# Kernel tuning notes

Measured on AMD Instinct MI355X. Metric: run time of the kernel, lower is better.

Reference implementation:

```python
import jax, jax.numpy as jnp
import numpy as np


def _avgpool(x, k):
    # x: (N, C, H, W), k divides H and W
    if k == 1:
        return x
    N, C, H, W = x.shape
    return x.reshape(N, C, H // k, k, W // k, k).mean(axis=(3, 5))


def _pairwise_sum(mu1, var1, mu2, var2):
    # mu*, var*: (N, D). Broadcast to (N, N, D), fused elementwise chain + full sum.
    d = mu1[:, None, :] - mu2[None, :, :]
    v = var1[:, None, :] + var2[None, :, :]
    return jnp.sum(jnp.exp(-0.5 * d * d / v) / jnp.sqrt(v))


def setup_inputs() -> dict:
    key = jax.random.key(0)
    k1, k2, k3, k4 = jax.random.split(key, 4)
    shape = (64, 16, 64, 64)
    return {
        "mu_a": jax.random.normal(k1, shape, dtype=jnp.float32),
        "logvar_a": jax.random.normal(k2, shape, dtype=jnp.float32),
        "mu_b": jax.random.normal(k3, shape, dtype=jnp.float32),
        "logvar_b": jax.random.normal(k4, shape, dtype=jnp.float32),
        "kern": 2,
    }


def reference(mu_a, logvar_a, mu_b, logvar_b, kern):
    k2 = float(kern * kern)
    mu_a_p = _avgpool(mu_a, kern)
    mu_b_p = _avgpool(mu_b, kern)
    var_a = _avgpool(jnp.exp(logvar_a), kern) / k2
    var_b = _avgpool(jnp.exp(logvar_b), kern) / k2

    N = mu_a_p.shape[0]
    mu_a_f = mu_a_p.reshape(N, -1)
    mu_b_f = mu_b_p.reshape(N, -1)
    var_a_f = var_a.reshape(N, -1)
    var_b_f = var_b.reshape(N, -1)

    vaa = _pairwise_sum(mu_a_f, var_a_f, mu_a_f, var_a_f)
    vab = _pairwise_sum(mu_a_f, var_a_f, mu_b_f, var_b_f)
    vbb = _pairwise_sum(mu_b_f, var_b_f, mu_b_f, var_b_f)
    return vaa + vbb - 2.0 * vab
```

## Files before the change

kernel.cpp:

```cpp
#include <hip/hip_runtime.h>

#define N_ 64
#define C_ 16
#define H_ 64
#define W_ 64

#define TRI_BLOCKS 288
#define PAIR_GROUPS (2 * TRI_BLOCKS + 512)
#define DSPLIT 4
#define PAIR_BLOCKS (PAIR_GROUPS * DSPLIT)


__global__ __launch_bounds__(256) void pool_kernel(
    const float* __restrict__ mu_a, const float* __restrict__ lv_a,
    const float* __restrict__ mu_b, const float* __restrict__ lv_b,
    const int* __restrict__ kern_p, float* __restrict__ ws,
    float* __restrict__ out) {
    if (blockIdx.x == 0 && threadIdx.x == 0) out[0] = 0.0f;

    const int k = kern_p[0];
    const float LOG2E = 1.44269504088896f;

    if (k == 2) {
        const int Np = (N_ * C_ * H_ * W_) >> 2;
        const int Q  = Np >> 2;
        const int total = 4 * Q;
        for (int g = blockIdx.x * blockDim.x + threadIdx.x; g < total;
             g += gridDim.x * blockDim.x) {
            const int a  = g >> 18;
            const int r4 = g & (Q - 1);
            const int pw4 = (r4 & 7) << 2;
            const int t   = r4 >> 3;
            const int ph  = t & 31;
            const int nc  = t >> 5;
            const float* src = (a == 0) ? mu_a : (a == 1) ? lv_a : (a == 2) ? mu_b : lv_b;
            const bool is_var = (a & 1);
            const float* p0 = src + nc * (H_ * W_) + (ph * 2) * W_ + pw4 * 2;
            float4 r0a = *(const float4*)(p0);
            float4 r0b = *(const float4*)(p0 + 4);
            float4 r1a = *(const float4*)(p0 + W_);
            float4 r1b = *(const float4*)(p0 + W_ + 4);
            float o0, o1, o2, o3;
            if (is_var) {
#define E_(x) __builtin_amdgcn_exp2f((x) * LOG2E)
                o0 = E_(r0a.x) + E_(r0a.y) + E_(r1a.x) + E_(r1a.y);
                o1 = E_(r0a.z) + E_(r0a.w) + E_(r1a.z) + E_(r1a.w);
                o2 = E_(r0b.x) + E_(r0b.y) + E_(r1b.x) + E_(r1b.y);
                o3 = E_(r0b.z) + E_(r0b.w) + E_(r1b.z) + E_(r1b.w);
#undef E_
                const float s = 1.0f / 16.0f;
                o0 *= s; o1 *= s; o2 *= s; o3 *= s;
            } else {
                o0 = r0a.x + r0a.y + r1a.x + r1a.y;
                o1 = r0a.z + r0a.w + r1a.z + r1a.w;
                o2 = r0b.x + r0b.y + r1b.x + r1b.y;
                o3 = r0b.z + r0b.w + r1b.z + r1b.w;
                const float s = 0.25f;
                o0 *= s; o1 *= s; o2 *= s; o3 *= s;
            }
            *(float4*)(ws + (size_t)a * Np + (size_t)r4 * 4) = make_float4(o0, o1, o2, o3);
        }
    } else {
        const int Hp = H_ / k, Wp = W_ / k;
        const int Np = N_ * C_ * Hp * Wp;
        const float inv_k2 = 1.0f / (float)(k * k);
        const float inv_k4 = inv_k2 * inv_k2;
        const int total = 4 * Np;
        for (int p = blockIdx.x * blockDim.x + threadIdx.x; p < total;
             p += gridDim.x * blockDim.x) {
            const int a  = p / Np;
            const int r  = p - a * Np;
            const int pw = r % Wp;
            const int t1 = r / Wp;
            const int ph = t1 % Hp;
            const int nc = t1 / Hp;
            const float* src = (a == 0) ? mu_a : (a == 1) ? lv_a : (a == 2) ? mu_b : lv_b;
            const bool is_var = (a & 1);
            const int base = nc * (H_ * W_) + (ph * k) * W_ + (pw * k);
            float s = 0.0f;
            for (int dy = 0; dy < k; ++dy) {
                const float* row = src + base + dy * W_;
                for (int dx = 0; dx < k; ++dx) {
                    float x = row[dx];
                    s += is_var ? __builtin_amdgcn_exp2f(x * LOG2E) : x;
                }
            }
            ws[(size_t)a * Np + r] = s * (is_var ? inv_k4 : inv_k2);
        }
    }
}

__global__ __launch_bounds__(256) void pair_kernel(const float* __restrict__ ws,
                                                   const int* __restrict__ kern_p,
                                                   float* __restrict__ out) {
    const int k = kern_p[0];
    const int D  = C_ * (H_ / k) * (W_ / k);
    const int Np = N_ * D;

    const float* mu_a = ws;
    const float* va   = ws + (size_t)Np;
    const float* mu_b = ws + (size_t)2 * Np;
    const float* vb   = ws + (size_t)3 * Np;

    const int pb = blockIdx.x >> 2;
    const int c  = blockIdx.x & 3;
    int set, i, jt;
    if (pb >= 2 * TRI_BLOCKS) {
        set = 2;
        const int t = pb - 2 * TRI_BLOCKS;
        i  = t >> 3;
        jt = t & 7;
    } else {
        set = (pb >= TRI_BLOCKS) ? 1 : 0;
        const int t = (pb >= TRI_BLOCKS) ? (pb - TRI_BLOCKS) : pb;
        int g = 0;
        while (g < 7 && 4 * (g + 1) * (g + 2) <= t) ++g;
        const int r = t - 4 * g * (g + 1);
        i  = 8 * g + r / (g + 1);
        jt = r % (g + 1);
    }

    const float *mu1, *v1, *mu2, *v2;
    if (set == 0)      { mu1 = mu2 = mu_a; v1 = v2 = va; }
    else if (set == 1) { mu1 = mu2 = mu_b; v1 = v2 = vb; }
    else               { mu1 = mu_a; v1 = va; mu2 = mu_b; v2 = vb; }

    const int j0 = jt * 8;
    float wgt[8];
    for (int j8 = 0; j8 < 8; ++j8) {
        if (set == 2) wgt[j8] = -2.0f;
        else {
            const int j = j0 + j8;
            wgt[j8] = (j > i) ? 0.0f : (j == i) ? 1.0f : 2.0f;
        }
    }

    const float NHALF_LOG2E = -0.721347520444482f;
#define TERM(mx1, sx1, mx2, sx2)                                       \
    {                                                                  \
        float v  = (sx1) + (sx2);                                      \
        float rs = __builtin_amdgcn_rsqf(v);                           \
        float d  = (mx1) - (mx2);                                      \
        float t_ = d * rs;                                             \
        float e  = __builtin_amdgcn_exp2f((NHALF_LOG2E * t_) * t_);    \
        a = fmaf(e, rs, a);                                            \
    }

    float accs[8] = {0, 0, 0, 0, 0, 0, 0, 0};

    if (D == 16384) {
        const int base = (c << 12) + (threadIdx.x << 2);
        const float* Mi = mu1 + (size_t)i * D + base;
        const float* Vi = v1  + (size_t)i * D + base;
        const float4 im0 = *(const float4*)(Mi);
        const float4 im1 = *(const float4*)(Mi + 1024);
        const float4 im2 = *(const float4*)(Mi + 2048);
        const float4 im3 = *(const float4*)(Mi + 3072);
        const float4 iv0 = *(const float4*)(Vi);
        const float4 iv1 = *(const float4*)(Vi + 1024);
        const float4 iv2 = *(const float4*)(Vi + 2048);
        const float4 iv3 = *(const float4*)(Vi + 3072);
        for (int j8 = 0; j8 < 8; ++j8) {
            const float* Mj = mu2 + (size_t)(j0 + j8) * D + base;
            const float* Vj = v2  + (size_t)(j0 + j8) * D + base;
            const float4 jm0 = *(const float4*)(Mj);
            const float4 jm1 = *(const float4*)(Mj + 1024);
            const float4 jm2 = *(const float4*)(Mj + 2048);
            const float4 jm3 = *(const float4*)(Mj + 3072);
            const float4 jv0 = *(const float4*)(Vj);
            const float4 jv1 = *(const float4*)(Vj + 1024);
            const float4 jv2 = *(const float4*)(Vj + 2048);
            const float4 jv3 = *(const float4*)(Vj + 3072);
            float a = 0.0f;
            TERM(im0.x, iv0.x, jm0.x, jv0.x) TERM(im0.y, iv0.y, jm0.y, jv0.y)
            TERM(im0.z, iv0.z, jm0.z, jv0.z) TERM(im0.w, iv0.w, jm0.w, jv0.w)
            TERM(im1.x, iv1.x, jm1.x, jv1.x) TERM(im1.y, iv1.y, jm1.y, jv1.y)
            TERM(im1.z, iv1.z, jm1.z, jv1.z) TERM(im1.w, iv1.w, jm1.w, jv1.w)
            TERM(im2.x, iv2.x, jm2.x, jv2.x) TERM(im2.y, iv2.y, jm2.y, jv2.y)
            TERM(im2.z, iv2.z, jm2.z, jv2.z) TERM(im2.w, iv2.w, jm2.w, jv2.w)
            TERM(im3.x, iv3.x, jm3.x, jv3.x) TERM(im3.y, iv3.y, jm3.y, jv3.y)
            TERM(im3.z, iv3.z, jm3.z, jv3.z) TERM(im3.w, iv3.w, jm3.w, jv3.w)
            accs[j8] += a;
        }
    } else {
        const int lo = (c * D) >> 2, hi = ((c + 1) * D) >> 2;
        const float* Mi = mu1 + (size_t)i * D;
        const float* Vi = v1  + (size_t)i * D;
        for (int j8 = 0; j8 < 8; ++j8) {
            const float* Mj = mu2 + (size_t)(j0 + j8) * D;
            const float* Vj = v2  + (size_t)(j0 + j8) * D;
            float a = 0.0f;
            for (int e = lo + (int)threadIdx.x; e < hi; e += 256) {
                TERM(Mi[e], Vi[e], Mj[e], Vj[e])
            }
            accs[j8] = a;
        }
    }
#undef TERM

    float tot = 0.0f;
    for (int j8 = 0; j8 < 8; ++j8) tot += wgt[j8] * accs[j8];

    for (int off = 32; off > 0; off >>= 1)
        tot += __shfl_down(tot, off, 64);
    __shared__ float wsum[4];
    const int lane = threadIdx.x & 63;
    const int wid  = threadIdx.x >> 6;
    if (lane == 0) wsum[wid] = tot;
    __syncthreads();
    if (threadIdx.x == 0) {
        atomicAdd(out, wsum[0] + wsum[1] + wsum[2] + wsum[3]);
    }
}

extern "C" void kernel_launch(void* const* d_in, const int* in_sizes, int n_in,
                              void* d_out, int out_size, void* d_ws, size_t ws_size,
                              hipStream_t stream) {
    const float* mu_a = (const float*)d_in[0];
    const float* lv_a = (const float*)d_in[1];
    const float* mu_b = (const float*)d_in[2];
    const float* lv_b = (const float*)d_in[3];
    const int*   kern = (const int*)d_in[4];
    float* out = (float*)d_out;
    float* ws  = (float*)d_ws;

    pool_kernel<<<4096, 256, 0, stream>>>(mu_a, lv_a, mu_b, lv_b, kern, ws, out);
    pair_kernel<<<PAIR_BLOCKS, 256, 0, stream>>>(ws, kern, out);
}
```

Baseline: 165.1 us.

## Tile pair kernel as 4x8 row blocks with finer D chunking

Reworks the pairwise kernel so each block computes a 4-row by 8-column tile of sample pairs over a 1024-element chunk of the feature dimension (16 chunks), in place of one row against 8 columns over a quarter of D. Each loaded j vector is reused across four i rows, which cuts global/L2 traffic per term, and the triangular tile enumeration is recomputed for 4x8 tiles. The cost is more accumulator registers (32 per thread) and some wasted work on diagonal tiles whose upper-triangle entries get zero weight.

```diff
diff --git a/kernel.cpp b/kernel.cpp
--- a/kernel.cpp
+++ b/kernel.cpp
@@ -5,10 +5,10 @@
 #define H_ 64
 #define W_ 64
 
-#define TRI_BLOCKS 288
-#define PAIR_GROUPS (2 * TRI_BLOCKS + 512)
-#define DSPLIT 4
-#define PAIR_BLOCKS (PAIR_GROUPS * DSPLIT)
+#define TRI_TILES 72
+#define TILES 272
+#define DCHUNKS 16
+#define PAIR_BLOCKS (TILES * DCHUNKS)
 
 
 __global__ __launch_bounds__(256) void pool_kernel(
@@ -102,104 +102,99 @@
     const float* mu_b = ws + (size_t)2 * Np;
     const float* vb   = ws + (size_t)3 * Np;
 
-    const int pb = blockIdx.x >> 2;
-    const int c  = blockIdx.x & 3;
-    int set, i, jt;
-    if (pb >= 2 * TRI_BLOCKS) {
+    const int c = blockIdx.x & (DCHUNKS - 1);
+    const int t = blockIdx.x >> 4;
+    int set, it, jt;
+    if (t >= 2 * TRI_TILES) {
         set = 2;
-        const int t = pb - 2 * TRI_BLOCKS;
-        i  = t >> 3;
-        jt = t & 7;
+        const int tt = t - 2 * TRI_TILES;
+        it = tt >> 3;
+        jt = tt & 7;
     } else {
-        set = (pb >= TRI_BLOCKS) ? 1 : 0;
-        const int t = (pb >= TRI_BLOCKS) ? (pb - TRI_BLOCKS) : pb;
-        int g = 0;
-        while (g < 7 && 4 * (g + 1) * (g + 2) <= t) ++g;
-        const int r = t - 4 * g * (g + 1);
-        i  = 8 * g + r / (g + 1);
-        jt = r % (g + 1);
-    }
+        set = (t >= TRI_TILES) ? 1 : 0;
+        const int tt = set ? (t - TRI_TILES) : t;
+        int g = 0, cum = 0;
+        while (cum + (g >> 1) + 1 <= tt) { cum += (g >> 1) + 1; ++g; }
+        it = g;
+        jt = tt - cum;
+    }
+    const int i0 = it * 4, j0 = jt * 8;
 
     const float *mu1, *v1, *mu2, *v2;
     if (set == 0)      { mu1 = mu2 = mu_a; v1 = v2 = va; }
     else if (set == 1) { mu1 = mu2 = mu_b; v1 = v2 = vb; }
     else               { mu1 = mu_a; v1 = va; mu2 = mu_b; v2 = vb; }
 
-    const int j0 = jt * 8;
-    float wgt[8];
-    for (int j8 = 0; j8 < 8; ++j8) {
-        if (set == 2) wgt[j8] = -2.0f;
-        else {
-            const int j = j0 + j8;
-            wgt[j8] = (j > i) ? 0.0f : (j == i) ? 1.0f : 2.0f;
-        }
-    }
-
     const float NHALF_LOG2E = -0.721347520444482f;
-#define TERM(mx1, sx1, mx2, sx2)                                       \
+#define TERM(acc, mx1, sx1, mx2, sx2)                                  \
     {                                                                  \
         float v  = (sx1) + (sx2);                                      \
         float rs = __builtin_amdgcn_rsqf(v);                           \
         float d  = (mx1) - (mx2);                                      \
         float t_ = d * rs;                                             \
         float e  = __builtin_amdgcn_exp2f((NHALF_LOG2E * t_) * t_);    \
-        a = fmaf(e, rs, a);                                            \
-    }
-
-    float accs[8] = {0, 0, 0, 0, 0, 0, 0, 0};
+        acc = fmaf(e, rs, acc);                                        \
+    }
+
+    float accs[4][8];
+    #pragma unroll
+    for (int ir = 0; ir < 4; ++ir)
+        #pragma unroll
+        for (int j8 = 0; j8 < 8; ++j8) accs[ir][j8] = 0.0f;
 
     if (D == 16384) {
-        const int base = (c << 12) + (threadIdx.x << 2);
-        const float* Mi = mu1 + (size_t)i * D + base;
-        const float* Vi = v1  + (size_t)i * D + base;
-        const float4 im0 = *(const float4*)(Mi);
-        const float4 im1 = *(const float4*)(Mi + 1024);
-        const float4 im2 = *(const float4*)(Mi + 2048);
-        const float4 im3 = *(const float4*)(Mi + 3072);
-        const float4 iv0 = *(const float4*)(Vi);
-        const float4 iv1 = *(const float4*)(Vi + 1024);
-        const float4 iv2 = *(const float4*)(Vi + 2048);
-        const float4 iv3 = *(const float4*)(Vi + 3072);
+        const int base = (c << 10) + ((int)threadIdx.x << 2);
+        float4 im[4], iv[4];
+        #pragma unroll
+        for (int ir = 0; ir < 4; ++ir) {
+            im[ir] = *(const float4*)(mu1 + (size_t)(i0 + ir) * 16384 + base);
+            iv[ir] = *(const float4*)(v1  + (size_t)(i0 + ir) * 16384 + base);
+        }
+        #pragma unroll
         for (int j8 = 0; j8 < 8; ++j8) {
-            const float* Mj = mu2 + (size_t)(j0 + j8) * D + base;
-            const float* Vj = v2  + (size_t)(j0 + j8) * D + base;
-            const float4 jm0 = *(const float4*)(Mj);
-            const float4 jm1 = *(const float4*)(Mj + 1024);
-            const float4 jm2 = *(const float4*)(Mj + 2048);
-            const float4 jm3 = *(const float4*)(Mj + 3072);
-            const float4 jv0 = *(const float4*)(Vj);
-            const float4 jv1 = *(const float4*)(Vj + 1024);
-            const float4 jv2 = *(const float4*)(Vj + 2048);
-            const float4 jv3 = *(const float4*)(Vj + 3072);
-            float a = 0.0f;
-            TERM(im0.x, iv0.x, jm0.x, jv0.x) TERM(im0.y, iv0.y, jm0.y, jv0.y)
-            TERM(im0.z, iv0.z, jm0.z, jv0.z) TERM(im0.w, iv0.w, jm0.w, jv0.w)
-            TERM(im1.x, iv1.x, jm1.x, jv1.x) TERM(im1.y, iv1.y, jm1.y, jv1.y)
-            TERM(im1.z, iv1.z, jm1.z, jv1.z) TERM(im1.w, iv1.w, jm1.w, jv1.w)
-            TERM(im2.x, iv2.x, jm2.x, jv2.x) TERM(im2.y, iv2.y, jm2.y, jv2.y)
-            TERM(im2.z, iv2.z, jm2.z, jv2.z) TERM(im2.w, iv2.w, jm2.w, jv2.w)
-            TERM(im3.x, iv3.x, jm3.x, jv3.x) TERM(im3.y, iv3.y, jm3.y, jv3.y)
-            TERM(im3.z, iv3.z, jm3.z, jv3.z) TERM(im3.w, iv3.w, jm3.w, jv3.w)
-            accs[j8] += a;
+            const float4 jm = *(const float4*)(mu2 + (size_t)(j0 + j8) * 16384 + base);
+            const float4 jv = *(const float4*)(v2  + (size_t)(j0 + j8) * 16384 + base);
+            #pragma unroll
+            for (int ir = 0; ir < 4; ++ir) {
+                TERM(accs[ir][j8], im[ir].x, iv[ir].x, jm.x, jv.x)
+                TERM(accs[ir][j8], im[ir].y, iv[ir].y, jm.y, jv.y)
+                TERM(accs[ir][j8], im[ir].z, iv[ir].z, jm.z, jv.z)
+                TERM(accs[ir][j8], im[ir].w, iv[ir].w, jm.w, jv.w)
+            }
         }
     } else {
-        const int lo = (c * D) >> 2, hi = ((c + 1) * D) >> 2;
-        const float* Mi = mu1 + (size_t)i * D;
-        const float* Vi = v1  + (size_t)i * D;
+        const int cs = D / DCHUNKS;
+        const int lo = c * cs, hi = lo + cs;
+        for (int e = lo + (int)threadIdx.x; e < hi; e += 256) {
+            #pragma unroll
+            for (int j8 = 0; j8 < 8; ++j8) {
+                const float mj = mu2[(size_t)(j0 + j8) * D + e];
+                const float vj = v2 [(size_t)(j0 + j8) * D + e];
+                #pragma unroll
+                for (int ir = 0; ir < 4; ++ir) {
+                    const float mi = mu1[(size_t)(i0 + ir) * D + e];
+                    const float vi = v1 [(size_t)(i0 + ir) * D + e];
+                    TERM(accs[ir][j8], mi, vi, mj, vj)
+                }
+            }
+        }
+    }
+#undef TERM
+
+    float tot = 0.0f;
+    #pragma unroll
+    for (int ir = 0; ir < 4; ++ir) {
+        #pragma unroll
         for (int j8 = 0; j8 < 8; ++j8) {
-            const float* Mj = mu2 + (size_t)(j0 + j8) * D;
-            const float* Vj = v2  + (size_t)(j0 + j8) * D;
-            float a = 0.0f;
-            for (int e = lo + (int)threadIdx.x; e < hi; e += 256) {
-                TERM(Mi[e], Vi[e], Mj[e], Vj[e])
-            }
-            accs[j8] = a;
-        }
-    }
-#undef TERM
-
-    float tot = 0.0f;
-    for (int j8 = 0; j8 < 8; ++j8) tot += wgt[j8] * accs[j8];
+            float w;
+            if (set == 2) w = -2.0f;
+            else {
+                const int ii = i0 + ir, jj = j0 + j8;
+                w = (jj > ii) ? 0.0f : (jj == ii) ? 1.0f : 2.0f;
+            }
+            tot = fmaf(w, accs[ir][j8], tot);
+        }
+    }
 
     for (int off = 32; off > 0; off >>= 1)
         tot += __shfl_down(tot, off, 64);
```

Measured after the change: 160.1 us. -3.0%, faster.
